# Performance work log

Hardware: AMD Instinct MI355X
Metric: run time of the kernel (lower is better)

Reference implementation:

```python
import jax, jax.numpy as jnp
import numpy as np

N = 16777216  # rows
G = 1024      # distinct group keys (power of 2 -> no binary-search padding)


def setup_inputs() -> dict:
    key = jax.random.key(0)
    k1, k2, k3 = jax.random.split(key, 3)
    # guarantee every group id in [0, G) appears at least once
    base = jnp.arange(G, dtype=jnp.int32)
    rest = jax.random.randint(k1, (N - G,), 0, G, dtype=jnp.int32)
    key_col = jax.random.permutation(k2, jnp.concatenate([base, rest])).reshape(-1, 1)
    val_col = jax.random.normal(k3, (N, 1), dtype=jnp.float32)
    return {"key_col": key_col, "val_col": val_col}


def _group_indices(x_flat, uniq_desc):
    # Faithful vectorized replication of find_mapping_indices: binary search of each
    # x against the reverse-sorted (descending) unique keys. G is a power of 2 so
    # N_prime == G and no front padding occurs.
    steps = int(np.log2(G))
    offset = G // 2
    pos = (x_flat <= uniq_desc[offset]).astype(jnp.int32) * offset
    offset = offset // 2  # int(ceil(offset/2)) == offset//2 for powers of two
    for _ in range(1, steps):
        bins = (x_flat <= uniq_desc[pos + offset]).astype(jnp.int32)
        pos = pos + bins * offset
        offset = offset // 2
    return pos  # [N] group index in [0, G)


def reference(key_col, val_col):
    x = key_col.reshape(-1)
    v = val_col.reshape(-1)
    # torch.sort(torch.unique(x), descending=True): all G values present by construction
    uniq_desc = jnp.unique(x, size=G)[::-1]
    gid = _group_indices(x, uniq_desc)
    # fused segmented reduces replace the per-group masked_select loop (same math)
    s = jax.ops.segment_sum(v, gid, num_segments=G)
    cnt = jax.ops.segment_sum(jnp.ones_like(v), gid, num_segments=G)
    avg = s / cnt  # torch.mean per group; every group non-empty
    mn = jax.ops.segment_min(v, gid, num_segments=G)
    mx = jax.ops.segment_max(v, gid, num_segments=G)
    # group_selection_mask is all-True (every group occupied) -> masked_select is identity
    key_out = uniq_desc.reshape(-1, 1)
    return (key_out,
            s.reshape(-1, 1),
            avg.reshape(-1, 1),
            mn.reshape(-1, 1),
            mx.reshape(-1, 1))
```

## Files before the change

### kernel.cpp

```cpp
#include <hip/hip_runtime.h>

#define G 1024
#define SCALEF 1048576.0f
#define CNT_SHIFT 42
#define ELEM_BIAS (1 << 24)
#define LOW_MASK ((1ULL << CNT_SHIFT) - 1)
#define GCNT_SHIFT 44
#define GSUM_BIAS (1ll << 23)
#define GLOW_MASK ((1ULL << GCNT_SHIFT) - 1)
#define NREP 64
#define NREP_MM 8

__device__ __forceinline__ unsigned omap(float x) {
    unsigned u = __float_as_uint(x);
    return (u & 0x80000000u) ? ~u : (u | 0x80000000u);
}
__device__ __forceinline__ float ounmap(unsigned o) {
    unsigned u = (o & 0x80000000u) ? (o & 0x7fffffffu) : ~o;
    return __uint_as_float(u);
}

__global__ __launch_bounds__(256) void gb_warm(
    const int4* __restrict__ keys, const float4* __restrict__ vals, int n4w,
    unsigned* __restrict__ rmaxo, unsigned* __restrict__ rminv)
{
    __shared__ unsigned s_mn[G];
    __shared__ unsigned s_mx[G];
    for (int k = threadIdx.x; k < G; k += 256) { s_mn[k] = 0xffffffffu; s_mx[k] = 0u; }
    __syncthreads();

    const int stride = gridDim.x * 256;
    for (int i = blockIdx.x * 256 + threadIdx.x; i < n4w; i += stride) {
        int4 k4 = keys[i]; float4 v4 = vals[i];
        unsigned o;
        o = omap(v4.x); atomicMin(&s_mn[k4.x], o); atomicMax(&s_mx[k4.x], o);
        o = omap(v4.y); atomicMin(&s_mn[k4.y], o); atomicMax(&s_mx[k4.y], o);
        o = omap(v4.z); atomicMin(&s_mn[k4.z], o); atomicMax(&s_mx[k4.z], o);
        o = omap(v4.w); atomicMin(&s_mn[k4.w], o); atomicMax(&s_mx[k4.w], o);
    }
    __syncthreads();

    const int r = blockIdx.x & (NREP_MM - 1);
    for (int k = threadIdx.x; k < G; k += 256) {
        const unsigned mn = s_mn[k], mx = s_mx[k];
        if (mn != 0xffffffffu) atomicMax(&rminv[r * G + k], ~mn);
        if (mx != 0u)          atomicMax(&rmaxo[r * G + k], mx);
    }
}

__global__ __launch_bounds__(1024) void gb_gate(
    const unsigned* __restrict__ rmaxo, const unsigned* __restrict__ rminv,
    unsigned* __restrict__ gate2)
{
    const int k = threadIdx.x;
    unsigned mx = 0u, mv = 0u;
    for (int r = 0; r < NREP_MM; ++r) {
        mx = max(mx, rmaxo[r * G + k]);
        mv = max(mv, rminv[r * G + k]);
    }
    __shared__ unsigned l_tmin[1024];
    __shared__ unsigned l_tmax[1024];
    l_tmin[k] = ~mv;
    l_tmax[k] = mx;
    __syncthreads();
    for (int s = 512; s > 0; s >>= 1) {
        if (k < s) {
            l_tmin[k] = max(l_tmin[k], l_tmin[k + s]);
            l_tmax[k] = min(l_tmax[k], l_tmax[k + s]);
        }
        __syncthreads();
    }
    if (k == 0) { gate2[0] = l_tmin[0]; gate2[1] = l_tmax[0]; }
}

__global__ __launch_bounds__(256) void gb_main(
    const int4* __restrict__ keys, const float4* __restrict__ vals, int n4,
    unsigned long long* __restrict__ racc,
    unsigned* __restrict__ rmaxo, unsigned* __restrict__ rminv,
    const unsigned* __restrict__ gate2)
{
    __shared__ unsigned long long s_sc[G];
    for (int k = threadIdx.x; k < G; k += 256) s_sc[k] = 0ull;

    const unsigned Tmin = gate2[0];
    const unsigned Tmax = gate2[1];
    __syncthreads();

    const int rmm = blockIdx.x & (NREP_MM - 1);
    unsigned* __restrict__ rmaxo_r = rmaxo + rmm * G;
    unsigned* __restrict__ rminv_r = rminv + rmm * G;

#define MAIN_ELEM(KK, VV)                                                      \
        {                                                                      \
            const int k = (KK); const float v = (VV);                          \
            const unsigned o = omap(v);                                        \
            if (o <= Tmin) atomicMax(&rminv_r[k], ~o);                         \
            if (o >= Tmax) atomicMax(&rmaxo_r[k], o);                          \
            const int vf = __float2int_rn(v * SCALEF);                         \
            atomicAdd(&s_sc[k], (1ULL << CNT_SHIFT) +                          \
                      (unsigned long long)(unsigned)(vf + ELEM_BIAS));         \
        }

    const int stride = gridDim.x * 256;
    int i = blockIdx.x * 256 + threadIdx.x;
    if (i < n4) {
        int4 k4 = keys[i]; float4 v4 = vals[i];
        for (i += stride; ; i += stride) {
            const bool more = (i < n4);
            int4 nk; float4 nv;
            if (more) { nk = keys[i]; nv = vals[i]; }
            MAIN_ELEM(k4.x, v4.x) MAIN_ELEM(k4.y, v4.y)
            MAIN_ELEM(k4.z, v4.z) MAIN_ELEM(k4.w, v4.w)
            if (!more) break;
            k4 = nk; v4 = nv;
        }
    }
#undef MAIN_ELEM
    __syncthreads();

    const int r = blockIdx.x & (NREP - 1);
    unsigned long long* __restrict__ racc_r = racc + r * G;
    for (int k = threadIdx.x; k < G; k += 256) {
        const unsigned long long cell = s_sc[k];
        const unsigned n = (unsigned)(cell >> CNT_SHIFT);
        if (n) {
            const long long s = (long long)(cell & LOW_MASK) - ((long long)n << 24);
            atomicAdd(&racc_r[k],
                      ((unsigned long long)n << GCNT_SHIFT) +
                      (unsigned long long)(s + (long long)n * GSUM_BIAS));
        }
    }
}

__global__ __launch_bounds__(256) void gb_write(
    const unsigned long long* __restrict__ racc,
    const unsigned* __restrict__ rmaxo, const unsigned* __restrict__ rminv,
    float* __restrict__ out)
{
    const int k = blockIdx.x * 256 + threadIdx.x;
    unsigned long long cell = 0ull;
    for (int r = 0; r < NREP; ++r) cell += racc[r * G + k];
    unsigned mx = 0u, mv = 0u;
    for (int r = 0; r < NREP_MM; ++r) {
        mx = max(mx, rmaxo[r * G + k]);
        mv = max(mv, rminv[r * G + k]);
    }
    const unsigned n = (unsigned)(cell >> GCNT_SHIFT);
    const long long s = (long long)(cell & GLOW_MASK) - (long long)n * GSUM_BIAS;
    const float sum = (float)((double)s * (1.0 / (double)SCALEF));
    const int g = (G - 1) - k;
    out[g]         = (float)k;
    out[G + g]     = sum;
    out[2 * G + g] = sum / (float)n;
    out[3 * G + g] = ounmap(~mv);
    out[4 * G + g] = ounmap(mx);
}

extern "C" void kernel_launch(void* const* d_in, const int* in_sizes, int n_in,
                              void* d_out, int out_size, void* d_ws, size_t ws_size,
                              hipStream_t stream) {
    const int4*   keys = (const int4*)d_in[0];
    const float4* vals = (const float4*)d_in[1];
    const int n   = in_sizes[0];
    const int n4  = n / 4;
    int n4w = n4 >> 4;
    if (n4w < 1)  n4w = (n4 < 1) ? 0 : n4;
    if (n4w > n4) n4w = n4;

    unsigned long long* racc  = (unsigned long long*)d_ws;
    unsigned*           rmaxo = (unsigned*)(racc + (size_t)NREP * G);
    unsigned*           rminv = rmaxo + (size_t)NREP_MM * G;
    unsigned*           gate2 = rminv + (size_t)NREP_MM * G;
    const size_t acc_bytes = (size_t)NREP * G * 8 + (size_t)NREP_MM * G * 8
                           + 2 * sizeof(unsigned);

    hipMemsetAsync(d_ws, 0, acc_bytes, stream);

    hipLaunchKernelGGL(gb_warm, dim3(512), dim3(256), 0, stream,
                       keys, vals, n4w, rmaxo, rminv);
    hipLaunchKernelGGL(gb_gate, dim3(1), dim3(1024), 0, stream,
                       rmaxo, rminv, gate2);
    hipLaunchKernelGGL(gb_main, dim3(2048), dim3(256), 0, stream,
                       keys, vals, n4, racc, rmaxo, rminv, gate2);
    hipLaunchKernelGGL(gb_write, dim3(G / 256), dim3(256), 0, stream,
                       racc, rmaxo, rminv, (float*)d_out);
}
```

Baseline: 168.6 us.

## Fuse min/max into main pass via shared-memory atomics, drop warm and gate kernels

Removes the warm-up sampling pass and the gate kernel that computed global thresholds for gating global min/max atomics. Min and max are now tracked per block in shared memory alongside the packed sum/count cell, then flushed once per group to 32 replicated global slots. This drops two launches and a partial extra read of the inputs, at the cost of two extra LDS atomics per element in the hot loop. Block size also changes from 256 to 512 threads with half as many blocks.

```diff
diff --git a/kernel.cpp b/kernel.cpp
--- a/kernel.cpp
+++ b/kernel.cpp
@@ -9,7 +9,7 @@
 #define GSUM_BIAS (1ll << 23)
 #define GLOW_MASK ((1ULL << GCNT_SHIFT) - 1)
 #define NREP 64
-#define NREP_MM 8
+#define NREP_MM 32
 
 __device__ __forceinline__ unsigned omap(float x) {
     unsigned u = __float_as_uint(x);
@@ -20,89 +20,32 @@
     return __uint_as_float(u);
 }
 
-__global__ __launch_bounds__(256) void gb_warm(
-    const int4* __restrict__ keys, const float4* __restrict__ vals, int n4w,
+__global__ __launch_bounds__(512) void gb_main(
+    const int4* __restrict__ keys, const float4* __restrict__ vals, int n4,
+    unsigned long long* __restrict__ racc,
     unsigned* __restrict__ rmaxo, unsigned* __restrict__ rminv)
 {
+    __shared__ unsigned long long s_sc[G];
     __shared__ unsigned s_mn[G];
     __shared__ unsigned s_mx[G];
-    for (int k = threadIdx.x; k < G; k += 256) { s_mn[k] = 0xffffffffu; s_mx[k] = 0u; }
-    __syncthreads();
-
-    const int stride = gridDim.x * 256;
-    for (int i = blockIdx.x * 256 + threadIdx.x; i < n4w; i += stride) {
-        int4 k4 = keys[i]; float4 v4 = vals[i];
-        unsigned o;
-        o = omap(v4.x); atomicMin(&s_mn[k4.x], o); atomicMax(&s_mx[k4.x], o);
-        o = omap(v4.y); atomicMin(&s_mn[k4.y], o); atomicMax(&s_mx[k4.y], o);
-        o = omap(v4.z); atomicMin(&s_mn[k4.z], o); atomicMax(&s_mx[k4.z], o);
-        o = omap(v4.w); atomicMin(&s_mn[k4.w], o); atomicMax(&s_mx[k4.w], o);
+    for (int k = threadIdx.x; k < G; k += 512) {
+        s_sc[k] = 0ull; s_mn[k] = 0xffffffffu; s_mx[k] = 0u;
     }
     __syncthreads();
-
-    const int r = blockIdx.x & (NREP_MM - 1);
-    for (int k = threadIdx.x; k < G; k += 256) {
-        const unsigned mn = s_mn[k], mx = s_mx[k];
-        if (mn != 0xffffffffu) atomicMax(&rminv[r * G + k], ~mn);
-        if (mx != 0u)          atomicMax(&rmaxo[r * G + k], mx);
-    }
-}
-
-__global__ __launch_bounds__(1024) void gb_gate(
-    const unsigned* __restrict__ rmaxo, const unsigned* __restrict__ rminv,
-    unsigned* __restrict__ gate2)
-{
-    const int k = threadIdx.x;
-    unsigned mx = 0u, mv = 0u;
-    for (int r = 0; r < NREP_MM; ++r) {
-        mx = max(mx, rmaxo[r * G + k]);
-        mv = max(mv, rminv[r * G + k]);
-    }
-    __shared__ unsigned l_tmin[1024];
-    __shared__ unsigned l_tmax[1024];
-    l_tmin[k] = ~mv;
-    l_tmax[k] = mx;
-    __syncthreads();
-    for (int s = 512; s > 0; s >>= 1) {
-        if (k < s) {
-            l_tmin[k] = max(l_tmin[k], l_tmin[k + s]);
-            l_tmax[k] = min(l_tmax[k], l_tmax[k + s]);
-        }
-        __syncthreads();
-    }
-    if (k == 0) { gate2[0] = l_tmin[0]; gate2[1] = l_tmax[0]; }
-}
-
-__global__ __launch_bounds__(256) void gb_main(
-    const int4* __restrict__ keys, const float4* __restrict__ vals, int n4,
-    unsigned long long* __restrict__ racc,
-    unsigned* __restrict__ rmaxo, unsigned* __restrict__ rminv,
-    const unsigned* __restrict__ gate2)
-{
-    __shared__ unsigned long long s_sc[G];
-    for (int k = threadIdx.x; k < G; k += 256) s_sc[k] = 0ull;
-
-    const unsigned Tmin = gate2[0];
-    const unsigned Tmax = gate2[1];
-    __syncthreads();
-
-    const int rmm = blockIdx.x & (NREP_MM - 1);
-    unsigned* __restrict__ rmaxo_r = rmaxo + rmm * G;
-    unsigned* __restrict__ rminv_r = rminv + rmm * G;
 
 #define MAIN_ELEM(KK, VV)                                                      \
         {                                                                      \
             const int k = (KK); const float v = (VV);                          \
             const unsigned o = omap(v);                                        \
-            if (o <= Tmin) atomicMax(&rminv_r[k], ~o);                         \
-            if (o >= Tmax) atomicMax(&rmaxo_r[k], o);                          \
+            atomicMin(&s_mn[k], o);                                            \
+            atomicMax(&s_mx[k], o);                                            \
             const int vf = __float2int_rn(v * SCALEF);                         \
             atomicAdd(&s_sc[k], (1ULL << CNT_SHIFT) +                          \
                       (unsigned long long)(unsigned)(vf + ELEM_BIAS));         \
         }
 
-    const int stride = gridDim.x * 256;
-    int i = blockIdx.x * 256 + threadIdx.x;
+    const int stride = gridDim.x * 512;
+    int i = blockIdx.x * 512 + threadIdx.x;
     if (i < n4) {
         int4 k4 = keys[i]; float4 v4 = vals[i];
         for (i += stride; ; i += stride) {
@@ -118,9 +61,12 @@
 #undef MAIN_ELEM
     __syncthreads();
 
-    const int r = blockIdx.x & (NREP - 1);
-    unsigned long long* __restrict__ racc_r = racc + r * G;
-    for (int k = threadIdx.x; k < G; k += 256) {
+    const int r  = blockIdx.x & (NREP - 1);
+    const int rm = blockIdx.x & (NREP_MM - 1);
+    unsigned long long* __restrict__ racc_r  = racc  + (size_t)r  * G;
+    unsigned*           __restrict__ rmaxo_r = rmaxo + (size_t)rm * G;
+    unsigned*           __restrict__ rminv_r = rminv + (size_t)rm * G;
+    for (int k = threadIdx.x; k < G; k += 512) {
         const unsigned long long cell = s_sc[k];
         const unsigned n = (unsigned)(cell >> CNT_SHIFT);
         if (n) {
@@ -128,6 +74,8 @@
             atomicAdd(&racc_r[k],
                       ((unsigned long long)n << GCNT_SHIFT) +
                       (unsigned long long)(s + (long long)n * GSUM_BIAS));
+            atomicMax(&rmaxo_r[k], s_mx[k]);
+            atomicMax(&rminv_r[k], ~s_mn[k]);
         }
     }
 }
@@ -161,27 +109,18 @@
                               hipStream_t stream) {
     const int4*   keys = (const int4*)d_in[0];
     const float4* vals = (const float4*)d_in[1];
-    const int n   = in_sizes[0];
-    const int n4  = n / 4;
-    int n4w = n4 >> 4;
-    if (n4w < 1)  n4w = (n4 < 1) ? 0 : n4;
-    if (n4w > n4) n4w = n4;
+    const int n  = in_sizes[0];
+    const int n4 = n / 4;
 
     unsigned long long* racc  = (unsigned long long*)d_ws;
     unsigned*           rmaxo = (unsigned*)(racc + (size_t)NREP * G);
     unsigned*           rminv = rmaxo + (size_t)NREP_MM * G;
-    unsigned*           gate2 = rminv + (size_t)NREP_MM * G;
-    const size_t acc_bytes = (size_t)NREP * G * 8 + (size_t)NREP_MM * G * 8
-                           + 2 * sizeof(unsigned);
+    const size_t acc_bytes = (size_t)NREP * G * 8 + 2 * (size_t)NREP_MM * G * 4;
 
     hipMemsetAsync(d_ws, 0, acc_bytes, stream);
 
-    hipLaunchKernelGGL(gb_warm, dim3(512), dim3(256), 0, stream,
-                       keys, vals, n4w, rmaxo, rminv);
-    hipLaunchKernelGGL(gb_gate, dim3(1), dim3(1024), 0, stream,
-                       rmaxo, rminv, gate2);
-    hipLaunchKernelGGL(gb_main, dim3(2048), dim3(256), 0, stream,
-                       keys, vals, n4, racc, rmaxo, rminv, gate2);
+    hipLaunchKernelGGL(gb_main, dim3(1024), dim3(512), 0, stream,
+                       keys, vals, n4, racc, rmaxo, rminv);
     hipLaunchKernelGGL(gb_write, dim3(G / 256), dim3(256), 0, stream,
                        racc, rmaxo, rminv, (float*)d_out);
 }
```

Measured after the change: 160.8 us. 1.05x faster.

## Privatize gated min/max in LDS and batch loads in main pass

Applied to the files above, without the earlier changes.

The main kernel now accumulates gated min/max candidates in shared-memory arrays instead of issuing global atomics per element, and flushes them once per block. It switches to 1024 blocks of 512 threads, and when the size divides exactly it issues all eight int4/float4 loads up front to raise memory-level parallelism. This cuts global atomic traffic and exposes more loads in flight, at the cost of more LDS per block and higher register pressure from the load buffers.

```diff
diff --git a/kernel.cpp b/kernel.cpp
--- a/kernel.cpp
+++ b/kernel.cpp
@@ -73,54 +73,72 @@
     if (k == 0) { gate2[0] = l_tmin[0]; gate2[1] = l_tmax[0]; }
 }
 
-__global__ __launch_bounds__(256) void gb_main(
+__global__ __launch_bounds__(512) void gb_main(
     const int4* __restrict__ keys, const float4* __restrict__ vals, int n4,
     unsigned long long* __restrict__ racc,
     unsigned* __restrict__ rmaxo, unsigned* __restrict__ rminv,
     const unsigned* __restrict__ gate2)
 {
     __shared__ unsigned long long s_sc[G];
-    for (int k = threadIdx.x; k < G; k += 256) s_sc[k] = 0ull;
-
+    __shared__ unsigned s_mn[G];
+    __shared__ unsigned s_mx[G];
+    for (int k = threadIdx.x; k < G; k += 512) {
+        s_sc[k] = 0ull; s_mn[k] = 0xffffffffu; s_mx[k] = 0u;
+    }
     const unsigned Tmin = gate2[0];
     const unsigned Tmax = gate2[1];
     __syncthreads();
 
-    const int rmm = blockIdx.x & (NREP_MM - 1);
-    unsigned* __restrict__ rmaxo_r = rmaxo + rmm * G;
-    unsigned* __restrict__ rminv_r = rminv + rmm * G;
-
 #define MAIN_ELEM(KK, VV)                                                      \
         {                                                                      \
-            const int k = (KK); const float v = (VV);                          \
-            const unsigned o = omap(v);                                        \
-            if (o <= Tmin) atomicMax(&rminv_r[k], ~o);                         \
-            if (o >= Tmax) atomicMax(&rmaxo_r[k], o);                          \
-            const int vf = __float2int_rn(v * SCALEF);                         \
-            atomicAdd(&s_sc[k], (1ULL << CNT_SHIFT) +                          \
+            const int mk = (KK); const float mv = (VV);                        \
+            const unsigned o = omap(mv);                                       \
+            if (o <= Tmin) atomicMin(&s_mn[mk], o);                            \
+            if (o >= Tmax) atomicMax(&s_mx[mk], o);                            \
+            const int vf = __float2int_rn(mv * SCALEF);                        \
+            atomicAdd(&s_sc[mk], (1ULL << CNT_SHIFT) +                         \
                       (unsigned long long)(unsigned)(vf + ELEM_BIAS));         \
         }
 
-    const int stride = gridDim.x * 256;
-    int i = blockIdx.x * 256 + threadIdx.x;
-    if (i < n4) {
-        int4 k4 = keys[i]; float4 v4 = vals[i];
-        for (i += stride; ; i += stride) {
-            const bool more = (i < n4);
-            int4 nk; float4 nv;
-            if (more) { nk = keys[i]; nv = vals[i]; }
-            MAIN_ELEM(k4.x, v4.x) MAIN_ELEM(k4.y, v4.y)
-            MAIN_ELEM(k4.z, v4.z) MAIN_ELEM(k4.w, v4.w)
-            if (!more) break;
-            k4 = nk; v4 = nv;
+    const int tid    = blockIdx.x * 512 + threadIdx.x;
+    const int stride = gridDim.x * 512;
+
+    if (n4 == (stride << 3)) {
+        int4   kb[8];
+        float4 vb[8];
+#pragma unroll
+        for (int j = 0; j < 8; ++j) kb[j] = keys[tid + j * stride];
+#pragma unroll
+        for (int j = 0; j < 8; ++j) vb[j] = vals[tid + j * stride];
+#pragma unroll
+        for (int j = 0; j < 8; ++j) {
+            MAIN_ELEM(kb[j].x, vb[j].x) MAIN_ELEM(kb[j].y, vb[j].y)
+            MAIN_ELEM(kb[j].z, vb[j].z) MAIN_ELEM(kb[j].w, vb[j].w)
+        }
+    } else {
+        int i = tid;
+        if (i < n4) {
+            int4 k4 = keys[i]; float4 v4 = vals[i];
+            for (i += stride; ; i += stride) {
+                const bool more = (i < n4);
+                int4 nk; float4 nv;
+                if (more) { nk = keys[i]; nv = vals[i]; }
+                MAIN_ELEM(k4.x, v4.x) MAIN_ELEM(k4.y, v4.y)
+                MAIN_ELEM(k4.z, v4.z) MAIN_ELEM(k4.w, v4.w)
+                if (!more) break;
+                k4 = nk; v4 = nv;
+            }
         }
     }
 #undef MAIN_ELEM
     __syncthreads();
 
-    const int r = blockIdx.x & (NREP - 1);
-    unsigned long long* __restrict__ racc_r = racc + r * G;
-    for (int k = threadIdx.x; k < G; k += 256) {
+    const int r  = blockIdx.x & (NREP - 1);
+    const int rm = blockIdx.x & (NREP_MM - 1);
+    unsigned long long* __restrict__ racc_r  = racc  + (size_t)r  * G;
+    unsigned*           __restrict__ rmaxo_r = rmaxo + (size_t)rm * G;
+    unsigned*           __restrict__ rminv_r = rminv + (size_t)rm * G;
+    for (int k = threadIdx.x; k < G; k += 512) {
         const unsigned long long cell = s_sc[k];
         const unsigned n = (unsigned)(cell >> CNT_SHIFT);
         if (n) {
@@ -129,6 +147,10 @@
                       ((unsigned long long)n << GCNT_SHIFT) +
                       (unsigned long long)(s + (long long)n * GSUM_BIAS));
         }
+        const unsigned mxv = s_mx[k];
+        const unsigned mnv = ~s_mn[k];
+        if (mxv) atomicMax(&rmaxo_r[k], mxv);
+        if (mnv) atomicMax(&rminv_r[k], mnv);
     }
 }
 
@@ -171,7 +193,7 @@
     unsigned*           rmaxo = (unsigned*)(racc + (size_t)NREP * G);
     unsigned*           rminv = rmaxo + (size_t)NREP_MM * G;
     unsigned*           gate2 = rminv + (size_t)NREP_MM * G;
-    const size_t acc_bytes = (size_t)NREP * G * 8 + (size_t)NREP_MM * G * 8
+    const size_t acc_bytes = (size_t)NREP * G * 8 + 2 * (size_t)NREP_MM * G * 4
                            + 2 * sizeof(unsigned);
 
     hipMemsetAsync(d_ws, 0, acc_bytes, stream);
@@ -180,7 +202,7 @@
                        keys, vals, n4w, rmaxo, rminv);
     hipLaunchKernelGGL(gb_gate, dim3(1), dim3(1024), 0, stream,
                        rmaxo, rminv, gate2);
-    hipLaunchKernelGGL(gb_main, dim3(2048), dim3(256), 0, stream,
+    hipLaunchKernelGGL(gb_main, dim3(1024), dim3(512), 0, stream,
                        keys, vals, n4, racc, rmaxo, rminv, gate2);
     hipLaunchKernelGGL(gb_write, dim3(G / 256), dim3(256), 0, stream,
                        racc, rmaxo, rminv, (float*)d_out);
```

Result: faster. 162.7 us (-3.5%).
